# Kernel tuning notes

Measured on AMD Instinct MI355X. Metric: run time of the kernel, lower is better.

## Reference

```python
import jax, jax.numpy as jnp
import numpy as np

T = 1024          # tokens (flattened batch*seq)
H = 1024          # hidden_size
NH = 8            # num_attention_heads
NKV = 4           # num_key_value_heads
HD = H // NH      # head_dim = 128
E = 32            # n_routed_experts
TOPK = 4          # num_experts_per_tok
NG = 8            # n_group
TKG = 4           # topk_group
MI = 512          # moe_intermediate_size
SI = MI * 2       # shared experts intermediate (n_shared_experts=2)
THETA = 10000.0
EPS = 1e-6
RSF = 2.5         # routed_scaling_factor


def setup_inputs() -> dict:
    key = jax.random.key(0)
    ks = jax.random.split(key, 16)
    s = jnp.float32(0.02)
    def nrm(k, shape):
        return jax.random.normal(k, shape, jnp.float32) * s
    return {
        "hidden_states": jax.random.normal(ks[0], (T, H), jnp.float32),
        "position_ids": jnp.arange(T, dtype=jnp.int32),
        "ln1_w": jnp.ones((H,), jnp.float32),
        "ln2_w": jnp.ones((H,), jnp.float32),
        "q_w": nrm(ks[1], (H, H)),            # torch Linear layout [out, in]
        "k_w": nrm(ks[2], (NKV * HD, H)),
        "v_w": nrm(ks[3], (NKV * HD, H)),
        "o_w": nrm(ks[4], (H, H)),
        "router_w": nrm(ks[5], (E, H)),
        "router_bias": jnp.zeros((E,), jnp.float32),  # e_score_correction_bias
        "eg_w": nrm(ks[6], (E, H, MI)),       # expert gate_proj, [E, in, out]
        "eu_w": nrm(ks[7], (E, H, MI)),       # expert up_proj
        "ed_w": nrm(ks[8], (E, MI, H)),       # expert down_proj
        "sg_w": nrm(ks[9], (H, SI)),          # shared experts gate_proj, [in, out]
        "su_w": nrm(ks[10], (H, SI)),
        "sd_w": nrm(ks[11], (SI, H)),
    }


def rmsnorm(x, w):
    var = jnp.mean(x * x, axis=-1, keepdims=True)
    return x * jax.lax.rsqrt(var + EPS) * w


def apply_rope(x, pos):
    # x: [T, heads, HD], non-interleaved (half-rotation)
    half = HD // 2
    inv_freq = 1.0 / (THETA ** (jnp.arange(half, dtype=jnp.float32) / half))
    freqs = pos.astype(jnp.float32)[:, None] * inv_freq[None, :]  # [T, half]
    cos = jnp.cos(freqs)[:, None, :]
    sin = jnp.sin(freqs)[:, None, :]
    x1, x2 = x[..., :half], x[..., half:]
    return jnp.concatenate([x1 * cos - x2 * sin, x2 * cos + x1 * sin], axis=-1)


def attention(h, pos, q_w, k_w, v_w, o_w):
    q = (h @ q_w.T).reshape(T, NH, HD)
    k = (h @ k_w.T).reshape(T, NKV, HD)
    v = (h @ v_w.T).reshape(T, NKV, HD)
    q = apply_rope(q, pos)
    k = apply_rope(k, pos)
    rep = NH // NKV
    k = jnp.repeat(k, rep, axis=1)  # [T, NH, HD]
    v = jnp.repeat(v, rep, axis=1)
    scale = 1.0 / np.sqrt(HD).astype(np.float32)
    scores = jnp.einsum("qhd,khd->hqk", q, k) * scale  # [NH, T, T]
    causal = jnp.tril(jnp.ones((T, T), bool))
    scores = jnp.where(causal[None], scores, jnp.finfo(scores.dtype).min)
    probs = jax.nn.softmax(scores, axis=-1)
    out = jnp.einsum("hqk,khd->qhd", probs, v).reshape(T, H)
    return out @ o_w.T


def router(x, router_w, router_bias):
    logits = x.astype(jnp.float32) @ router_w.T  # [T, E]
    scores = jax.nn.sigmoid(logits)
    sfc = scores + router_bias[None, :]
    # group-limited routing: sum of top-2 per group
    group_scores = jax.lax.top_k(sfc.reshape(T, NG, E // NG), 2)[0].sum(-1)  # [T, NG]
    gidx = jax.lax.top_k(group_scores, TKG)[1]  # [T, TKG]
    gmask = jnp.zeros((T, NG), jnp.float32).at[jnp.arange(T)[:, None], gidx].set(1.0)
    smask = jnp.repeat(gmask, E // NG, axis=1) > 0  # [T, E]
    masked = jnp.where(smask, sfc, 0.0)
    topk_idx = jax.lax.top_k(masked, TOPK)[1]  # [T, TOPK]
    topk_w = jnp.take_along_axis(scores, topk_idx, axis=1)
    topk_w = topk_w / (topk_w.sum(-1, keepdims=True) + 1e-20)  # norm_topk_prob
    return topk_idx, topk_w * RSF


def moe(x, router_w, router_bias, eg_w, eu_w, ed_w, sg_w, su_w, sd_w):
    topk_idx, topk_w = router(x, router_w, router_bias)
    # combine weights [T, E]
    cw = jnp.zeros((T, E), jnp.float32).at[jnp.arange(T)[:, None], topk_idx].add(topk_w)
    g = jnp.einsum("th,ehi->eti", x, eg_w)
    u = jnp.einsum("th,ehi->eti", x, eu_w)
    a = jax.nn.silu(g) * u
    o = jnp.einsum("eti,eih->eth", a, ed_w)
    routed = jnp.einsum("eth,te->th", o, cw)
    shared = (jax.nn.silu(x @ sg_w) * (x @ su_w)) @ sd_w
    return routed + shared


def reference(hidden_states, position_ids, ln1_w, ln2_w, q_w, k_w, v_w, o_w,
              router_w, router_bias, eg_w, eu_w, ed_w, sg_w, su_w, sd_w):
    res = hidden_states
    h = rmsnorm(hidden_states, ln1_w)
    h = attention(h, position_ids, q_w, k_w, v_w, o_w)
    h = res + h
    res = h
    h = rmsnorm(h, ln2_w)
    h = moe(h, router_w, router_bias, eg_w, eu_w, ed_w, sg_w, su_w, sd_w)
    return h + res
```

## Files before the change

### kernel.cpp

```cpp
#include <hip/hip_runtime.h>
#include <math.h>

#define T 1024
#define H 1024
#define NH 8
#define NKV 4
#define HD 128
#define NE 32
#define TOPK 4
#define NG 8
#define MI 512
#define SI 1024
#define RSF 2.5f
#define EPS 1e-6f

#define ASPLIT 4
#define SPLITK 256
#define NPSLOT 40

typedef short bf16x8 __attribute__((ext_vector_type(8)));
typedef float f32x4 __attribute__((ext_vector_type(4)));
#define MFMA16(a, b, c) __builtin_amdgcn_mfma_f32_16x16x32_bf16((a), (b), (c), 0, 0, 0)

__device__ inline unsigned short f2bf(float x) {
    unsigned u = __float_as_uint(x);
    u += 0x7fff + ((u >> 16) & 1);
    return (unsigned short)(u >> 16);
}
__device__ inline float bf2f(unsigned short h) { return __uint_as_float(((unsigned)h) << 16); }

__device__ __host__ inline int cqb_of(int qb) {
    int a = qb >> 2, r = qb & 3;
    return (a + 1) * (2 * a + r);
}

union U16S {
    unsigned short s[16];
    uint4 q[2];
};

__device__ __forceinline__ void gl16(const void* g, void* l) {
    __builtin_amdgcn_global_load_lds((const __attribute__((address_space(1))) unsigned int*)g,
                                     (__attribute__((address_space(3))) unsigned int*)l, 16, 0, 0);
}

__global__ void rmsnorm_split_kernel(const float* __restrict__ x, const float* __restrict__ w,
                                     unsigned short* __restrict__ oh,
                                     unsigned short* __restrict__ ol) {
    int t = blockIdx.x;
    __shared__ float red[256];
    const float* xr = x + (size_t)t * H;
    float s = 0.f;
    for (int i = threadIdx.x; i < H; i += 256) { float v = xr[i]; s += v * v; }
    red[threadIdx.x] = s;
    __syncthreads();
    for (int st = 128; st > 0; st >>= 1) {
        if (threadIdx.x < st) red[threadIdx.x] += red[threadIdx.x + st];
        __syncthreads();
    }
    float inv = rsqrtf(red[0] / (float)H + EPS);
    for (int i = threadIdx.x; i < H; i += 256) {
        float v = xr[i] * inv * w[i];
        unsigned short hb = f2bf(v);
        oh[(size_t)t * H + i] = hb;
        ol[(size_t)t * H + i] = f2bf(v - bf2f(hb));
    }
}

__global__ void rmsnorm_dual_kernel(const float* __restrict__ x, const float* __restrict__ w,
                                    float* __restrict__ outf, unsigned short* __restrict__ outb) {
    int t = blockIdx.x;
    __shared__ float red[256];
    const float* xr = x + (size_t)t * H;
    float s = 0.f;
    for (int i = threadIdx.x; i < H; i += 256) { float v = xr[i]; s += v * v; }
    red[threadIdx.x] = s;
    __syncthreads();
    for (int st = 128; st > 0; st >>= 1) {
        if (threadIdx.x < st) red[threadIdx.x] += red[threadIdx.x + st];
        __syncthreads();
    }
    float inv = rsqrtf(red[0] / (float)H + EPS);
    for (int i = threadIdx.x; i < H; i += 256) {
        float v = xr[i] * inv * w[i];
        outf[(size_t)t * H + i] = v;
        outb[(size_t)t * H + i] = f2bf(v);
    }
}

__global__ void split_w4(const float* __restrict__ qw, const float* __restrict__ kw,
                         const float* __restrict__ vw, const float* __restrict__ ow,
                         unsigned short* __restrict__ qh, unsigned short* __restrict__ ql,
                         unsigned short* __restrict__ kh, unsigned short* __restrict__ kl,
                         unsigned short* __restrict__ vh, unsigned short* __restrict__ vl,
                         unsigned short* __restrict__ oh, unsigned short* __restrict__ ol) {
    int z = blockIdx.z;
    const float* src;
    unsigned short *dh, *dl;
    int n;
    if (z == 0) { src = qw; dh = qh; dl = ql; n = H * H; }
    else if (z == 1) { src = kw; dh = kh; dl = kl; n = NKV * HD * H; }
    else if (z == 2) { src = vw; dh = vh; dl = vl; n = NKV * HD * H; }
    else { src = ow; dh = oh; dl = ol; n = H * H; }
    int i = (blockIdx.x * 256 + threadIdx.x) * 4;
    if (i >= n) return;
    float4 val = *(const float4*)&src[i];
    float vv[4] = {val.x, val.y, val.z, val.w};
    unsigned short hs[4], ls[4];
#pragma unroll
    for (int j = 0; j < 4; ++j) {
        hs[j] = f2bf(vv[j]);
        ls[j] = f2bf(vv[j] - bf2f(hs[j]));
    }
    uint2 hp, lp;
    hp.x = (unsigned)hs[0] | ((unsigned)hs[1] << 16);
    hp.y = (unsigned)hs[2] | ((unsigned)hs[3] << 16);
    lp.x = (unsigned)ls[0] | ((unsigned)ls[1] << 16);
    lp.y = (unsigned)ls[2] | ((unsigned)ls[3] << 16);
    *(uint2*)&dh[i] = hp;
    *(uint2*)&dl[i] = lp;
}

__global__ __launch_bounds__(256) void transpose_cvt(const float* __restrict__ W,
                                                     unsigned short* __restrict__ Wt, int K,
                                                     int N, int eoff) {
    int zl = blockIdx.z;
    const float* src = W + (size_t)(eoff + zl) * K * N;
    unsigned short* dst = Wt + (size_t)zl * K * N;
    int k0 = blockIdx.y * 64, n0 = blockIdx.x * 64;
    __shared__ unsigned short Ls[64][70];
    int tid = threadIdx.x;
    int nn = (tid & 15) * 4, kr = tid >> 4;
#pragma unroll
    for (int p = 0; p < 4; ++p) {
        int k = kr + p * 16;
        float4 v = *(const float4*)&src[(size_t)(k0 + k) * N + n0 + nn];
        Ls[k][nn] = f2bf(v.x);
        Ls[k][nn + 1] = f2bf(v.y);
        Ls[k][nn + 2] = f2bf(v.z);
        Ls[k][nn + 3] = f2bf(v.w);
    }
    __syncthreads();
    int n = tid >> 2, kq = (tid & 3) * 16;
    U16S o;
#pragma unroll
    for (int j = 0; j < 16; ++j) o.s[j] = Ls[kq + j][n];
    unsigned short* drow = dst + (size_t)(n0 + n) * K + k0 + kq;
    *(uint4*)drow = o.q[0];
    *(uint4*)(drow + 8) = o.q[1];
}

__global__ __launch_bounds__(256) void vt_split(const float* __restrict__ vb,
                                                unsigned short* __restrict__ VTh,
                                                unsigned short* __restrict__ VTl) {
    int t0 = blockIdx.x * 64, c0 = blockIdx.y * 64;
    __shared__ unsigned short Hs[64][70], Lsh[64][70];
    int tid = threadIdx.x;
    int nn = (tid & 15) * 4, kr = tid >> 4;
#pragma unroll
    for (int p = 0; p < 4; ++p) {
        int t = kr + p * 16;
        float4 v = *(const float4*)&vb[(size_t)(t0 + t) * (NKV * HD) + c0 + nn];
        float vv[4] = {v.x, v.y, v.z, v.w};
#pragma unroll
        for (int j = 0; j < 4; ++j) {
            unsigned short hb = f2bf(vv[j]);
            Hs[t][nn + j] = hb;
            Lsh[t][nn + j] = f2bf(vv[j] - bf2f(hb));
        }
    }
    __syncthreads();
    int n = tid >> 2, kq = (tid & 3) * 16;
    U16S oh, ol;
#pragma unroll
    for (int j = 0; j < 16; ++j) {
        oh.s[j] = Hs[kq + j][n];
        ol.s[j] = Lsh[kq + j][n];
    }
    size_t drow = (size_t)(c0 + n) * T + t0 + kq;
    *(uint4*)&VTh[drow] = oh.q[0];
    *(uint4*)&VTh[drow + 8] = oh.q[1];
    *(uint4*)&VTl[drow] = ol.q[0];
    *(uint4*)&VTl[drow + 8] = ol.q[1];
}

__global__ __launch_bounds__(256) void router_logits_kernel(const float* __restrict__ x,
                                                            const float* __restrict__ W,
                                                            float* __restrict__ logits) {
    int t = blockIdx.x;
    __shared__ float xs[H];
    int tid = threadIdx.x;
    *(float4*)&xs[tid * 4] = *(const float4*)&x[(size_t)t * H + tid * 4];
    __syncthreads();
    int e = tid >> 3, p = tid & 7;
    const float* wr = W + (size_t)e * H;
    float s = 0.f;
#pragma unroll
    for (int i = 0; i < 32; ++i) {
        int k = i * 32 + p * 4;
        float4 wv = *(const float4*)&wr[k];
        float4 xv = *(const float4*)&xs[k];
        s += wv.x * xv.x + wv.y * xv.y + wv.z * xv.z + wv.w * xv.w;
    }
#pragma unroll
    for (int off = 1; off < 8; off <<= 1) s += __shfl_xor(s, off);
    if (p == 0) logits[(size_t)t * NE + e] = s;
}

__global__ __launch_bounds__(256) void gemm3_qkv(
    const unsigned short* __restrict__ Xh, const unsigned short* __restrict__ Xl,
    const unsigned short* __restrict__ Wqh, const unsigned short* __restrict__ Wql,
    const unsigned short* __restrict__ Wkh, const unsigned short* __restrict__ Wkl,
    const unsigned short* __restrict__ Wvh, const unsigned short* __restrict__ Wvl,
    float* __restrict__ qo, float* __restrict__ ko, float* __restrict__ vo) {
    __shared__ short Ahs[2][128][32], Als[2][128][32], Bhs[2][64][32], Bls[2][64][32];
    int tid = threadIdx.x;
    int m0 = blockIdx.y * 128;
    int n0 = blockIdx.x * 64;
    const unsigned short *Wh, *Wl;
    float* O;
    int ldo, nc0;
    if (n0 < 1024) { nc0 = n0; Wh = Wqh; Wl = Wql; O = qo; ldo = H; }
    else if (n0 < 1536) { nc0 = n0 - 1024; Wh = Wkh; Wl = Wkl; O = ko; ldo = NKV * HD; }
    else { nc0 = n0 - 1536; Wh = Wvh; Wl = Wvl; O = vo; ldo = NKV * HD; }
    int wave = tid >> 6, lane = tid & 63;
    int lr = lane & 15, lq = lane >> 4;
    int wm = (wave >> 1) * 64, wn = (wave & 1) * 32;
    int srow = lane >> 2, skb = (lane & 3) * 8;
    const unsigned short *ah_p[2], *al_p[2];
#pragma unroll
    for (int p = 0; p < 2; ++p) {
        int m = m0 + wave * 32 + p * 16 + srow;
        ah_p[p] = Xh + (size_t)m * H + skb;
        al_p[p] = Xl + (size_t)m * H + skb;
    }
    int bn = nc0 + wave * 16 + srow;
    const unsigned short* bh_p = Wh + (size_t)bn * H + skb;
    const unsigned short* bl_p = Wl + (size_t)bn * H + skb;
    f32x4 acc[4][2];
#pragma unroll
    for (int i = 0; i < 4; ++i)
#pragma unroll
        for (int j = 0; j < 2; ++j) acc[i][j] = (f32x4){0.f, 0.f, 0.f, 0.f};
    for (int k0 = 0; k0 < H; k0 += 64) {
#pragma unroll
        for (int c = 0; c < 2; ++c) {
            int kc = k0 + c * 32;
#pragma unroll
            for (int p = 0; p < 2; ++p) {
                gl16(ah_p[p] + kc, &Ahs[c][wave * 32 + p * 16 + srow][skb]);
                gl16(al_p[p] + kc, &Als[c][wave * 32 + p * 16 + srow][skb]);
            }
            gl16(bh_p + kc, &Bhs[c][wave * 16 + srow][skb]);
            gl16(bl_p + kc, &Bls[c][wave * 16 + srow][skb]);
        }
        __syncthreads();
#pragma unroll
        for (int c = 0; c < 2; ++c) {
            bf16x8 a_h[4], a_l[4], b_h[2], b_l[2];
#pragma unroll
            for (int mt = 0; mt < 4; ++mt) {
                a_h[mt] = *(const bf16x8*)&Ahs[c][wm + mt * 16 + lr][lq * 8];
                a_l[mt] = *(const bf16x8*)&Als[c][wm + mt * 16 + lr][lq * 8];
            }
#pragma unroll
            for (int nt = 0; nt < 2; ++nt) {
                b_h[nt] = *(const bf16x8*)&Bhs[c][wn + nt * 16 + lr][lq * 8];
                b_l[nt] = *(const bf16x8*)&Bls[c][wn + nt * 16 + lr][lq * 8];
            }
#pragma unroll
            for (int mt = 0; mt < 4; ++mt)
#pragma unroll
                for (int nt = 0; nt < 2; ++nt) {
                    acc[mt][nt] = MFMA16(a_h[mt], b_h[nt], acc[mt][nt]);
                    acc[mt][nt] = MFMA16(a_h[mt], b_l[nt], acc[mt][nt]);
                    acc[mt][nt] = MFMA16(a_l[mt], b_h[nt], acc[mt][nt]);
                }
        }
        __syncthreads();
    }
#pragma unroll
    for (int mt = 0; mt < 4; ++mt)
#pragma unroll
        for (int nt = 0; nt < 2; ++nt)
#pragma unroll
            for (int p = 0; p < 4; ++p) {
                int m = m0 + wm + mt * 16 + lq * 4 + p;
                int col = nc0 + wn + nt * 16 + lr;
                O[(size_t)m * ldo + col] = acc[mt][nt][p];
            }
}

__global__ __launch_bounds__(256) void gemm3_res(
    const unsigned short* __restrict__ Agh, const unsigned short* __restrict__ Agl,
    const unsigned short* __restrict__ Wh, const unsigned short* __restrict__ Wl,
    const float* __restrict__ res, float* __restrict__ O) {
    __shared__ short Ahs[2][128][32], Als[2][128][32], Bhs[2][64][32], Bls[2][64][32];
    int tid = threadIdx.x;
    int m0 = blockIdx.y * 128;
    int n0 = blockIdx.x * 64;
    int wave = tid >> 6, lane = tid & 63;
    int lr = lane & 15, lq = lane >> 4;
    int wm = (wave >> 1) * 64, wn = (wave & 1) * 32;
    int srow = lane >> 2, skb = (lane & 3) * 8;
    const unsigned short *ah_p[2], *al_p[2];
#pragma unroll
    for (int p = 0; p < 2; ++p) {
        int m = m0 + wave * 32 + p * 16 + srow;
        ah_p[p] = Agh + (size_t)m * H + skb;
        al_p[p] = Agl + (size_t)m * H + skb;
    }
    int bn = n0 + wave * 16 + srow;
    const unsigned short* bh_p = Wh + (size_t)bn * H + skb;
    const unsigned short* bl_p = Wl + (size_t)bn * H + skb;
    f32x4 acc[4][2];
#pragma unroll
    for (int i = 0; i < 4; ++i)
#pragma unroll
        for (int j = 0; j < 2; ++j) acc[i][j] = (f32x4){0.f, 0.f, 0.f, 0.f};
    for (int k0 = 0; k0 < H; k0 += 64) {
#pragma unroll
        for (int c = 0; c < 2; ++c) {
            int kc = k0 + c * 32;
#pragma unroll
            for (int p = 0; p < 2; ++p) {
                gl16(ah_p[p] + kc, &Ahs[c][wave * 32 + p * 16 + srow][skb]);
                gl16(al_p[p] + kc, &Als[c][wave * 32 + p * 16 + srow][skb]);
            }
            gl16(bh_p + kc, &Bhs[c][wave * 16 + srow][skb]);
            gl16(bl_p + kc, &Bls[c][wave * 16 + srow][skb]);
        }
        __syncthreads();
#pragma unroll
        for (int c = 0; c < 2; ++c) {
            bf16x8 a_h[4], a_l[4], b_h[2], b_l[2];
#pragma unroll
            for (int mt = 0; mt < 4; ++mt) {
                a_h[mt] = *(const bf16x8*)&Ahs[c][wm + mt * 16 + lr][lq * 8];
                a_l[mt] = *(const bf16x8*)&Als[c][wm + mt * 16 + lr][lq * 8];
            }
#pragma unroll
            for (int nt = 0; nt < 2; ++nt) {
                b_h[nt] = *(const bf16x8*)&Bhs[c][wn + nt * 16 + lr][lq * 8];
                b_l[nt] = *(const bf16x8*)&Bls[c][wn + nt * 16 + lr][lq * 8];
            }
#pragma unroll
            for (int mt = 0; mt < 4; ++mt)
#pragma unroll
                for (int nt = 0; nt < 2; ++nt) {
                    acc[mt][nt] = MFMA16(a_h[mt], b_h[nt], acc[mt][nt]);
                    acc[mt][nt] = MFMA16(a_h[mt], b_l[nt], acc[mt][nt]);
                    acc[mt][nt] = MFMA16(a_l[mt], b_h[nt], acc[mt][nt]);
                }
        }
        __syncthreads();
    }
#pragma unroll
    for (int mt = 0; mt < 4; ++mt)
#pragma unroll
        for (int nt = 0; nt < 2; ++nt)
#pragma unroll
            for (int p = 0; p < 4; ++p) {
                int m = m0 + wm + mt * 16 + lq * 4 + p;
                int col = n0 + wn + nt * 16 + lr;
                O[(size_t)m * H + col] = res[(size_t)m * H + col] + acc[mt][nt][p];
            }
}

__global__ void rope_kernel(float* __restrict__ q, const float* __restrict__ k,
                            const int* __restrict__ pos, unsigned short* __restrict__ Khg,
                            unsigned short* __restrict__ Klg) {
    int i = blockIdx.x * 256 + threadIdx.x;
    const int totq = T * NH * 64;
    const int tot = totq + T * NKV * 64;
    if (i >= tot) return;
    if (i < totq) {
        int r = i;
        int d = r & 63; r >>= 6;
        int hh = r % NH, t = r / NH;
        float p = (float)pos[t];
        float inv = powf(10000.0f, -(float)d / 64.0f);
        float fr = p * inv;
        float sv, cv;
        sincosf(fr, &sv, &cv);
        size_t bi = ((size_t)t * NH + hh) * HD + d;
        float x1 = q[bi], x2 = q[bi + 64];
        q[bi] = x1 * cv - x2 * sv;
        q[bi + 64] = x2 * cv + x1 * sv;
    } else {
        int r = i - totq;
        int d = r & 63; r >>= 6;
        int hh = r % NKV, t = r / NKV;
        float p = (float)pos[t];
        float inv = powf(10000.0f, -(float)d / 64.0f);
        float fr = p * inv;
        float sv, cv;
        sincosf(fr, &sv, &cv);
        size_t bi = ((size_t)t * NKV + hh) * HD + d;
        float x1 = k[bi], x2 = k[bi + 64];
        float n1 = x1 * cv - x2 * sv;
        float n2 = x2 * cv + x1 * sv;
        unsigned short h1 = f2bf(n1), h2b = f2bf(n2);
        Khg[bi] = h1;
        Khg[bi + 64] = h2b;
        Klg[bi] = f2bf(n1 - bf2f(h1));
        Klg[bi + 64] = f2bf(n2 - bf2f(h2b));
    }
}

#define KS_LD 136
#define VS_LD 40
#define PS_LD 34
__global__ __launch_bounds__(256) void attn_split(const float* __restrict__ Q,
                                                  const unsigned short* __restrict__ Khg,
                                                  const unsigned short* __restrict__ Klg,
                                                  const unsigned short* __restrict__ VTh,
                                                  const unsigned short* __restrict__ VTl,
                                                  float* __restrict__ po,
                                                  float* __restrict__ pm,
                                                  float* __restrict__ pl) {
    int h = blockIdx.x;
    int qb = blockIdx.y;
    int sp = blockIdx.z;
    int kvh = h >> 1;
    int q0 = qb * 64;
    int kend = q0 + 64;
    int ks = sp * SPLITK;
    if (ks >= kend) return;
    int ke = min(ks + SPLITK, kend);
    __shared__ __attribute__((aligned(16))) short Ksh[32][KS_LD], Ksl[32][KS_LD];
    __shared__ __attribute__((aligned(16))) short Vsh[128][VS_LD], Vsl[128][VS_LD];
    __shared__ short Ph[4][16][PS_LD], Pl[4][16][PS_LD];
    int tid = threadIdx.x;
    int wave = tid >> 6, lane = tid & 63;
    int lr = lane & 15, lq = lane >> 4;
    const float scale = 0.08838834764831845f;

    bf16x8 qh[4], ql[4];
    {
        const float* qrow = Q + (size_t)(q0 + wave * 16 + lr) * H + h * HD;
#pragma unroll
        for (int c = 0; c < 4; ++c) {
            float4 v0 = *(const float4*)(qrow + c * 32 + lq * 8);
            float4 v1 = *(const float4*)(qrow + c * 32 + lq * 8 + 4);
            float vv[8] = {v0.x, v0.y, v0.z, v0.w, v1.x, v1.y, v1.z, v1.w};
#pragma unroll
            for (int j = 0; j < 8; ++j) {
                unsigned short hb = f2bf(vv[j]);
                qh[c][j] = (short)hb;
                ql[c][j] = (short)f2bf(vv[j] - bf2f(hb));
            }
        }
    }
    f32x4 o[8];
#pragma unroll
    for (int nt = 0; nt < 8; ++nt) o[nt] = (f32x4){0.f, 0.f, 0.f, 0.f};
    float m_r[4] = {-1e30f, -1e30f, -1e30f, -1e30f};
    float l_r[4] = {0.f, 0.f, 0.f, 0.f};

    int kts = ks >> 5, kte = ke >> 5;
    int ntw = ((q0 + wave * 16 + 15) >> 5) + 1;

    int key_k = tid >> 3, kc = (tid & 7) * 16;
    int d_v = tid >> 1, vc = (tid & 1) * 16;
    const unsigned short* kbase_h = Khg + (size_t)kvh * HD + kc;
    const unsigned short* kbase_l = Klg + (size_t)kvh * HD + kc;
    const unsigned short* vbase_h = VTh + (size_t)(kvh * HD + d_v) * T + vc;
    const unsigned short* vbase_l = VTl + (size_t)(kvh * HD + d_v) * T + vc;

    uint4 kr0, kr1, kr2, kr3, vr0, vr1, vr2, vr3;
#define LOADT(KT)                                                                    \
    {                                                                                \
        size_t koff = (size_t)((KT)*32 + key_k) * (NKV * HD);                        \
        kr0 = *(const uint4*)(kbase_h + koff);                                       \
        kr1 = *(const uint4*)(kbase_h + koff + 8);                                   \
        kr2 = *(const uint4*)(kbase_l + koff);                                       \
        kr3 = *(const uint4*)(kbase_l + koff + 8);                                   \
        int voff = (KT)*32;                                                          \
        vr0 = *(const uint4*)(vbase_h + voff);                                       \
        vr1 = *(const uint4*)(vbase_h + voff + 8);                                   \
        vr2 = *(const uint4*)(vbase_l + voff);                                       \
        vr3 = *(const uint4*)(vbase_l + voff + 8);                                   \
    }

    LOADT(kts);
    for (int kt = kts; kt < kte; ++kt) {
        int k0 = kt * 32;
        __syncthreads();
        *(uint4*)&Ksh[key_k][kc] = kr0;
        *(uint4*)&Ksh[key_k][kc + 8] = kr1;
        *(uint4*)&Ksl[key_k][kc] = kr2;
        *(uint4*)&Ksl[key_k][kc + 8] = kr3;
        *(uint4*)&Vsh[d_v][vc] = vr0;
        *(uint4*)&Vsh[d_v][vc + 8] = vr1;
        *(uint4*)&Vsl[d_v][vc] = vr2;
        *(uint4*)&Vsl[d_v][vc + 8] = vr3;
        __syncthreads();
        if (kt + 1 < kte) LOADT(kt + 1);
        if (kt < ntw) {
            f32x4 s[2];
            s[0] = (f32x4){0.f, 0.f, 0.f, 0.f};
            s[1] = (f32x4){0.f, 0.f, 0.f, 0.f};
#pragma unroll
            for (int nt = 0; nt < 2; ++nt)
#pragma unroll
                for (int c = 0; c < 4; ++c) {
                    bf16x8 kh = *(const bf16x8*)&Ksh[nt * 16 + lr][c * 32 + lq * 8];
                    bf16x8 kl = *(const bf16x8*)&Ksl[nt * 16 + lr][c * 32 + lq * 8];
                    s[nt] = MFMA16(qh[c], kh, s[nt]);
                    s[nt] = MFMA16(ql[c], kh, s[nt]);
                    s[nt] = MFMA16(qh[c], kl, s[nt]);
                }
            int gr_base = q0 + wave * 16 + lq * 4;
#pragma unroll
            for (int nt = 0; nt < 2; ++nt) {
                int gc = k0 + nt * 16 + lr;
#pragma unroll
                for (int p = 0; p < 4; ++p) {
                    float sv = s[nt][p] * scale;
                    if (gc > gr_base + p) sv = -1e30f;
                    s[nt][p] = sv;
                }
            }
            float alpha[4];
#pragma unroll
            for (int p = 0; p < 4; ++p) {
                float mx = fmaxf(s[0][p], s[1][p]);
#pragma unroll
                for (int off = 1; off < 16; off <<= 1) mx = fmaxf(mx, __shfl_xor(mx, off));
                float mn = fmaxf(m_r[p], mx);
                alpha[p] = __expf(m_r[p] - mn);
                float p0 = __expf(s[0][p] - mn);
                float p1 = __expf(s[1][p] - mn);
                float ps = p0 + p1;
#pragma unroll
                for (int off = 1; off < 16; off <<= 1) ps += __shfl_xor(ps, off);
                l_r[p] = l_r[p] * alpha[p] + ps;
                m_r[p] = mn;
                int r = lq * 4 + p;
                unsigned short h0 = f2bf(p0);
                Ph[wave][r][lr] = (short)h0;
                Pl[wave][r][lr] = (short)f2bf(p0 - bf2f(h0));
                unsigned short h1 = f2bf(p1);
                Ph[wave][r][lr + 16] = (short)h1;
                Pl[wave][r][lr + 16] = (short)f2bf(p1 - bf2f(h1));
            }
            bf16x8 pah = *(const bf16x8*)&Ph[wave][lr][lq * 8];
            bf16x8 pal = *(const bf16x8*)&Pl[wave][lr][lq * 8];
#pragma unroll
            for (int nt = 0; nt < 8; ++nt) {
#pragma unroll
                for (int p = 0; p < 4; ++p) o[nt][p] *= alpha[p];
                bf16x8 vh = *(const bf16x8*)&Vsh[nt * 16 + lr][lq * 8];
                bf16x8 vl = *(const bf16x8*)&Vsl[nt * 16 + lr][lq * 8];
                o[nt] = MFMA16(pah, vh, o[nt]);
                o[nt] = MFMA16(pal, vh, o[nt]);
                o[nt] = MFMA16(pah, vl, o[nt]);
            }
        }
    }
#undef LOADT
    int pbase = h * NPSLOT + cqb_of(qb) + sp;
    float* porow = po + (size_t)pbase * (64 * 128);
#pragma unroll
    for (int nt = 0; nt < 8; ++nt)
#pragma unroll
        for (int p = 0; p < 4; ++p) {
            int row = wave * 16 + lq * 4 + p;
            porow[row * 128 + nt * 16 + lr] = o[nt][p];
        }
    if (lr == 0) {
#pragma unroll
        for (int p = 0; p < 4; ++p) {
            int row = wave * 16 + lq * 4 + p;
            pm[(size_t)pbase * 64 + row] = m_r[p];
            pl[(size_t)pbase * 64 + row] = l_r[p];
        }
    }
}

__global__ __launch_bounds__(256) void attn_merge(const float* __restrict__ po,
                                                  const float* __restrict__ pm,
                                                  const float* __restrict__ pl,
                                                  unsigned short* __restrict__ Oh,
                                                  unsigned short* __restrict__ Ol) {
    int h = blockIdx.x, qb = blockIdx.y;
    int nact = qb / 4 + 1;
    int tid = threadIdx.x;
    int row = tid >> 2;
    int c0 = (tid & 3) * 32;
    int pb = h * NPSLOT + cqb_of(qb);
    float ms[ASPLIT], ws[ASPLIT];
    float mstar = -1e30f;
#pragma unroll
    for (int s = 0; s < ASPLIT; ++s)
        if (s < nact) {
            ms[s] = pm[(size_t)(pb + s) * 64 + row];
            mstar = fmaxf(mstar, ms[s]);
        }
    float lstar = 0.f;
#pragma unroll
    for (int s = 0; s < ASPLIT; ++s)
        if (s < nact) {
            ws[s] = __expf(ms[s] - mstar);
            lstar += ws[s] * pl[(size_t)(pb + s) * 64 + row];
        }
    float linv = 1.f / lstar;
    size_t obase = (size_t)(qb * 64 + row) * H + h * HD + c0;
#pragma unroll
    for (int j = 0; j < 32; j += 4) {
        float acc[4] = {0.f, 0.f, 0.f, 0.f};
#pragma unroll
        for (int s = 0; s < ASPLIT; ++s)
            if (s < nact) {
                float4 v =
                    *(const float4*)&po[(size_t)(pb + s) * (64 * 128) + row * 128 + c0 + j];
                acc[0] += ws[s] * v.x;
                acc[1] += ws[s] * v.y;
                acc[2] += ws[s] * v.z;
                acc[3] += ws[s] * v.w;
            }
#pragma unroll
        for (int q = 0; q < 4; ++q) {
            float v = acc[q] * linv;
            unsigned short hb = f2bf(v);
            Oh[obase + j + q] = hb;
            Ol[obase + j + q] = f2bf(v - bf2f(hb));
        }
    }
}

__global__ void router_kernel(const float* __restrict__ logits, const float* __restrict__ bias,
                              int* __restrict__ topk_idx, float* __restrict__ topkw) {
    int t = blockIdx.x * 256 + threadIdx.x;
    if (t >= T) return;
    float sc[NE], sfc[NE];
    for (int e = 0; e < NE; ++e) {
        float s = 1.f / (1.f + expf(-logits[(size_t)t * NE + e]));
        sc[e] = s;
        sfc[e] = s + bias[e];
    }
    float gs[NG];
    for (int g = 0; g < NG; ++g) {
        float m1 = -1e30f, m2 = -1e30f;
        for (int i = 0; i < 4; ++i) {
            float v = sfc[g * 4 + i];
            if (v > m1) { m2 = m1; m1 = v; }
            else if (v > m2) m2 = v;
        }
        gs[g] = m1 + m2;
    }
    bool gmask[NG];
    for (int g = 0; g < NG; ++g) gmask[g] = false;
    for (int r = 0; r < 4; ++r) {
        int bi = 0; float bv = -1e30f;
        for (int g = 0; g < NG; ++g)
            if (gs[g] > bv) { bv = gs[g]; bi = g; }
        gmask[bi] = true;
        gs[bi] = -1e30f;
    }
    float msfc[NE];
    for (int e = 0; e < NE; ++e) msfc[e] = gmask[e >> 2] ? sfc[e] : 0.f;
    int idx[TOPK]; float w[TOPK]; float wsum = 0.f;
    for (int r = 0; r < TOPK; ++r) {
        int bi = 0; float bv = -1e30f;
        for (int e = 0; e < NE; ++e)
            if (msfc[e] > bv) { bv = msfc[e]; bi = e; }
        idx[r] = bi;
        msfc[bi] = -1e30f;
        w[r] = sc[bi];
        wsum += w[r];
    }
    float inv = RSF / (wsum + 1e-20f);
    for (int r = 0; r < TOPK; ++r) {
        topk_idx[(size_t)t * TOPK + r] = idx[r];
        topkw[(size_t)t * TOPK + r] = w[r] * inv;
    }
}

__global__ void bucket_kernel(const int* __restrict__ topk_idx, int* __restrict__ counts,
                              int* __restrict__ offs, int* __restrict__ tok_of,
                              int* __restrict__ slot_of) {
    __shared__ int cnt[NE], off[NE], fil[NE];
    int tid = threadIdx.x;
    if (tid < NE) { cnt[tid] = 0; fil[tid] = 0; }
    __syncthreads();
    for (int i = tid; i < T * TOPK; i += 256) atomicAdd(&cnt[topk_idx[i]], 1);
    __syncthreads();
    if (tid == 0) {
        int a = 0;
        for (int e = 0; e < NE; ++e) { off[e] = a; a += cnt[e]; }
    }
    __syncthreads();
    if (tid < NE) { counts[tid] = cnt[tid]; offs[tid] = off[tid]; }
    for (int i = tid; i < T * TOPK; i += 256) {
        int e = topk_idx[i];
        int p = off[e] + atomicAdd(&fil[e], 1);
        tok_of[p] = i >> 2;
        slot_of[i] = p;
    }
}

__global__ __launch_bounds__(256) void up_mfma2(
    const unsigned short* __restrict__ Xb, const unsigned short* __restrict__ Gt,
    const unsigned short* __restrict__ Ut, size_t wstride, const int* __restrict__ tok_of,
    const int* __restrict__ offs, const int* __restrict__ counts, int eoff,
    unsigned short* __restrict__ outb, int ldo) {
    int zl = blockIdx.z;
    int e = eoff + zl;
    int cnt = counts ? counts[e] : T;
    int base = offs ? offs[e] : 0;
    int m0 = blockIdx.y * 128;
    if (m0 >= cnt) return;
    int n0 = blockIdx.x * 64;
    const unsigned short* gt = Gt + (size_t)zl * wstride;
    const unsigned short* ut = Ut + (size_t)zl * wstride;
    __shared__ short As[2][128][32];
    __shared__ short Gs[2][64][32];
    __shared__ short Us[2][64][32];
    __shared__ int toks[128];
    int tid = threadIdx.x;
    if (tid < 128) {
        int m = m0 + tid;
        if (m >= cnt) m = cnt - 1;
        toks[tid] = tok_of ? tok_of[base + m] : m;
    }
    __syncthreads();
    int wave = tid >> 6, lane = tid & 63;
    int lr = lane & 15, lq = lane >> 4;
    int wm = (wave >> 1) * 64, wn = (wave & 1) * 32;
    int srow = lane >> 2, skb = (lane & 3) * 8;
    const unsigned short* aptr[2];
#pragma unroll
    for (int p = 0; p < 2; ++p)
        aptr[p] = Xb + (size_t)toks[wave * 32 + p * 16 + srow] * H + skb;
    const unsigned short* gptr = gt + (size_t)(n0 + wave * 16 + srow) * H + skb;
    const unsigned short* uptr = ut + (size_t)(n0 + wave * 16 + srow) * H + skb;
    f32x4 ag[4][2], au[4][2];
#pragma unroll
    for (int i = 0; i < 4; ++i)
#pragma unroll
        for (int j = 0; j < 2; ++j) {
            ag[i][j] = (f32x4){0.f, 0.f, 0.f, 0.f};
            au[i][j] = (f32x4){0.f, 0.f, 0.f, 0.f};
        }
    for (int k0 = 0; k0 < H; k0 += 64) {
#pragma unroll
        for (int c = 0; c < 2; ++c) {
            int kc = k0 + c * 32;
#pragma unroll
            for (int p = 0; p < 2; ++p)
                gl16(aptr[p] + kc, &As[c][wave * 32 + p * 16 + srow][skb]);
            gl16(gptr + kc, &Gs[c][wave * 16 + srow][skb]);
            gl16(uptr + kc, &Us[c][wave * 16 + srow][skb]);
        }
        __syncthreads();
#pragma unroll
        for (int c = 0; c < 2; ++c) {
            bf16x8 a[4], gg[2], uu[2];
#pragma unroll
            for (int mt = 0; mt < 4; ++mt)
                a[mt] = *(const bf16x8*)&As[c][wm + mt * 16 + lr][lq * 8];
#pragma unroll
            for (int nt = 0; nt < 2; ++nt) {
                gg[nt] = *(const bf16x8*)&Gs[c][wn + nt * 16 + lr][lq * 8];
                uu[nt] = *(const bf16x8*)&Us[c][wn + nt * 16 + lr][lq * 8];
            }
#pragma unroll
            for (int mt = 0; mt < 4; ++mt)
#pragma unroll
                for (int nt = 0; nt < 2; ++nt) {
                    ag[mt][nt] = MFMA16(a[mt], gg[nt], ag[mt][nt]);
                    au[mt][nt] = MFMA16(a[mt], uu[nt], au[mt][nt]);
                }
        }
        __syncthreads();
    }
#pragma unroll
    for (int mt = 0; mt < 4; ++mt)
#pragma unroll
        for (int nt = 0; nt < 2; ++nt)
#pragma unroll
            for (int p = 0; p < 4; ++p) {
                int m = m0 + wm + mt * 16 + lq * 4 + p;
                if (m >= cnt) continue;
                int orow = tok_of ? base + m : m;
                int col = n0 + wn + nt * 16 + lr;
                float gv = ag[mt][nt][p], uv = au[mt][nt][p];
                float sv = gv / (1.f + __expf(-gv)) * uv;
                outb[(size_t)orow * ldo + col] = f2bf(sv);
            }
}

__global__ __launch_bounds__(256) void down_mfma2(const unsigned short* __restrict__ Ab, int K,
                                                  const unsigned short* __restrict__ Wt,
                                                  size_t wstride, const int* __restrict__ offs,
                                                  const int* __restrict__ counts, int eoff,
                                                  float* __restrict__ Co) {
    int zl = blockIdx.z;
    int e = eoff + zl;
    int cnt = counts ? counts[e] : T;
    int base = offs ? offs[e] : 0;
    int m0 = blockIdx.y * 128;
    if (m0 >= cnt) return;
    int n0 = blockIdx.x * 128;
    const unsigned short* wt = Wt + (size_t)zl * wstride;
    __shared__ short As[2][128][32];
    __shared__ short Bs[2][128][32];
    int tid = threadIdx.x;
    int wave = tid >> 6, lane = tid & 63;
    int lr = lane & 15, lq = lane >> 4;
    int wm = (wave >> 1) * 64, wn = (wave & 1) * 64;
    int srow = lane >> 2, skb = (lane & 3) * 8;
    const unsigned short* aptr[2];
    const unsigned short* bptr[2];
#pragma unroll
    for (int p = 0; p < 2; ++p) {
        int m = m0 + wave * 32 + p * 16 + srow;
        if (m >= cnt) m = cnt - 1;
        aptr[p] = Ab + (size_t)(base + m) * K + skb;
        bptr[p] = wt + (size_t)(n0 + wave * 32 + p * 16 + srow) * K + skb;
    }
    f32x4 acc[4][4];
#pragma unroll
    for (int i = 0; i < 4; ++i)
#pragma unroll
        for (int j = 0; j < 4; ++j) acc[i][j] = (f32x4){0.f, 0.f, 0.f, 0.f};
    for (int k0 = 0; k0 < K; k0 += 64) {
#pragma unroll
        for (int c = 0; c < 2; ++c) {
            int kc = k0 + c * 32;
#pragma unroll
            for (int p = 0; p < 2; ++p) {
                gl16(aptr[p] + kc, &As[c][wave * 32 + p * 16 + srow][skb]);
                gl16(bptr[p] + kc, &Bs[c][wave * 32 + p * 16 + srow][skb]);
            }
        }
        __syncthreads();
#pragma unroll
        for (int c = 0; c < 2; ++c) {
            bf16x8 a[4], b[4];
#pragma unroll
            for (int mt = 0; mt < 4; ++mt)
                a[mt] = *(const bf16x8*)&As[c][wm + mt * 16 + lr][lq * 8];
#pragma unroll
            for (int nt = 0; nt < 4; ++nt)
                b[nt] = *(const bf16x8*)&Bs[c][wn + nt * 16 + lr][lq * 8];
#pragma unroll
            for (int mt = 0; mt < 4; ++mt)
#pragma unroll
                for (int nt = 0; nt < 4; ++nt) acc[mt][nt] = MFMA16(a[mt], b[nt], acc[mt][nt]);
        }
        __syncthreads();
    }
#pragma unroll
    for (int mt = 0; mt < 4; ++mt)
#pragma unroll
        for (int nt = 0; nt < 4; ++nt)
#pragma unroll
            for (int p = 0; p < 4; ++p) {
                int m = m0 + wm + mt * 16 + lq * 4 + p;
                if (m >= cnt) continue;
                int col = n0 + wn + nt * 16 + lr;
                Co[(size_t)(base + m) * H + col] = acc[mt][nt][p];
            }
}

__global__ void combine_kernel(const float* __restrict__ o_slot, const int* __restrict__ slot_of,
                               const float* __restrict__ topkw, const float* __restrict__ h2,
                               const float* __restrict__ sharedo, float* __restrict__ out) {
    int t = blockIdx.x;
    int d = threadIdx.x * 4;
    float4 a = *(const float4*)&h2[(size_t)t * H + d];
    float4 b = *(const float4*)&sharedo[(size_t)t * H + d];
    float4 acc = make_float4(a.x + b.x, a.y + b.y, a.z + b.z, a.w + b.w);
#pragma unroll
    for (int r = 0; r < TOPK; ++r) {
        int s = slot_of[t * TOPK + r];
        float w = topkw[t * TOPK + r];
        float4 v = *(const float4*)&o_slot[(size_t)s * H + d];
        acc.x += w * v.x; acc.y += w * v.y; acc.z += w * v.z; acc.w += w * v.w;
    }
    *(float4*)&out[(size_t)t * H + d] = acc;
}

extern "C" void kernel_launch(void* const* d_in, const int* in_sizes, int n_in,
                              void* d_out, int out_size, void* d_ws, size_t ws_size,
                              hipStream_t stream) {
    const float* hidden = (const float*)d_in[0];
    const int* pos = (const int*)d_in[1];
    const float* ln1w = (const float*)d_in[2];
    const float* ln2w = (const float*)d_in[3];
    const float* q_w = (const float*)d_in[4];
    const float* k_w = (const float*)d_in[5];
    const float* v_w = (const float*)d_in[6];
    const float* o_w = (const float*)d_in[7];
    const float* router_w = (const float*)d_in[8];
    const float* router_b = (const float*)d_in[9];
    const float* eg_w = (const float*)d_in[10];
    const float* eu_w = (const float*)d_in[11];
    const float* ed_w = (const float*)d_in[12];
    const float* sg_w = (const float*)d_in[13];
    const float* su_w = (const float*)d_in[14];
    const float* sd_w = (const float*)d_in[15];
    float* out = (float*)d_out;

    float* f = (float*)d_ws;
    float* xslot = f;   f += (size_t)T * H;
    float* qb = f;      f += (size_t)T * H;
    float* kb = f;      f += (size_t)T * NKV * HD;
    float* vb = f;      f += (size_t)T * NKV * HD;
    float* aoslot = f;  f += (size_t)T * H;
    float* ext = f;     f += (size_t)4 * 1024 * 1024;
    float* h2 = f;      f += (size_t)T * H;
    float* h_ln2f = f;  f += (size_t)T * H;
    float* logits = f;  f += (size_t)T * NE;
    float* topkw = f;   f += (size_t)T * TOPK;
    float* o_slot = f;  f += (size_t)T * TOPK * H;
    float* sharedo = f; f += (size_t)T * H;
    unsigned short* h_ln2b = (unsigned short*)f;
    unsigned short* abuf = h_ln2b + (size_t)T * H;
    unsigned short* ashared = abuf + (size_t)T * TOPK * MI;
    int* topk_idx = (int*)(ashared + (size_t)T * SI);
    int* counts = topk_idx + T * TOPK;
    int* fills = counts + NE;
    int* offs = fills + NE;
    int* tok_of = offs + NE;
    int* slot_of = tok_of + T * TOPK;
    (void)fills;

    unsigned short* wT = (unsigned short*)((char*)d_ws + (size_t)80 * 1024 * 1024);
    unsigned short* egTall = wT;
    unsigned short* euTall = egTall + (size_t)NE * H * MI;
    unsigned short* edTall = euTall + (size_t)NE * H * MI;
    bool big_ws = ws_size >= (size_t)(80 + 96 + 1) * 1024 * 1024;

    unsigned short* We = (unsigned short*)ext;
    const size_t HH = (size_t)H * H;
    const size_t KH = (size_t)NKV * HD * H;
    unsigned short* Wqh = We;
    unsigned short* Wql = Wqh + HH;
    unsigned short* Wkh = Wql + HH;
    unsigned short* Wkl = Wkh + KH;
    unsigned short* Wvh = Wkl + KH;
    unsigned short* Wvl = Wvh + KH;
    unsigned short* Woh = Wvl + KH;
    unsigned short* Wol = Woh + HH;

    unsigned short* Xh = (unsigned short*)xslot;
    unsigned short* Xl = Xh + (size_t)T * H;
    unsigned short* Aoh = (unsigned short*)aoslot;
    unsigned short* Aol = Aoh + (size_t)T * H;

    unsigned short* Khg = (unsigned short*)xslot;
    unsigned short* Klg = Khg + (size_t)T * NKV * HD;
    unsigned short* VTh = Klg + (size_t)T * NKV * HD;
    unsigned short* VTl = VTh + (size_t)T * NKV * HD;

    float* attn_po = o_slot;
    float* attn_pm = (float*)abuf;
    float* attn_pl = attn_pm + (size_t)NH * NPSLOT * 64;

    unsigned short* arena = (unsigned short*)xslot;
    unsigned short* egT = arena;
    unsigned short* euT = arena + (size_t)16 * H * MI;
    unsigned short* edT = arena;
    unsigned short* sgT = arena;
    unsigned short* suT = arena + (size_t)H * SI;
    unsigned short* sdT = arena;

    dim3 b256(256);

    split_w4<<<dim3(HH / (256 * 4), 1, 4), b256, 0, stream>>>(q_w, k_w, v_w, o_w, Wqh, Wql,
                                                              Wkh, Wkl, Wvh, Wvl, Woh, Wol);
    rmsnorm_split_kernel<<<T, b256, 0, stream>>>(hidden, ln1w, Xh, Xl);

    gemm3_qkv<<<dim3(32, 8), b256, 0, stream>>>(Xh, Xl, Wqh, Wql, Wkh, Wkl, Wvh, Wvl,
                                                qb, kb, vb);
    {
        int tot = T * NH * 64 + T * NKV * 64;
        rope_kernel<<<(tot + 255) / 256, b256, 0, stream>>>(qb, kb, pos, Khg, Klg);
    }
    vt_split<<<dim3(T / 64, (NKV * HD) / 64), b256, 0, stream>>>(vb, VTh, VTl);
    attn_split<<<dim3(NH, T / 64, ASPLIT), b256, 0, stream>>>(qb, Khg, Klg, VTh, VTl,
                                                              attn_po, attn_pm, attn_pl);
    attn_merge<<<dim3(NH, T / 64), b256, 0, stream>>>(attn_po, attn_pm, attn_pl, Aoh, Aol);
    gemm3_res<<<dim3(16, 8), b256, 0, stream>>>(Aoh, Aol, Woh, Wol, hidden, h2);
    rmsnorm_dual_kernel<<<T, b256, 0, stream>>>(h2, ln2w, h_ln2f, h_ln2b);

    router_logits_kernel<<<T, b256, 0, stream>>>(h_ln2f, router_w, logits);
    router_kernel<<<(T + 255) / 256, b256, 0, stream>>>(logits, router_b, topk_idx, topkw);
    bucket_kernel<<<1, b256, 0, stream>>>(topk_idx, counts, offs, tok_of, slot_of);

    if (big_ws) {
        transpose_cvt<<<dim3(MI / 64, H / 64, NE), b256, 0, stream>>>(eg_w, egTall, H, MI, 0);
        transpose_cvt<<<dim3(MI / 64, H / 64, NE), b256, 0, stream>>>(eu_w, euTall, H, MI, 0);
        up_mfma2<<<dim3(MI / 64, 8, NE), b256, 0, stream>>>(
            h_ln2b, egTall, euTall, (size_t)H * MI, tok_of, offs, counts, 0, abuf, MI);
        transpose_cvt<<<dim3(H / 64, MI / 64, NE), b256, 0, stream>>>(ed_w, edTall, MI, H, 0);
        down_mfma2<<<dim3(H / 128, 8, NE), b256, 0, stream>>>(
            abuf, MI, edTall, (size_t)MI * H, offs, counts, 0, o_slot);
    } else {
        for (int g = 0; g < 2; ++g) {
            int eo = g * 16;
            transpose_cvt<<<dim3(MI / 64, H / 64, 16), b256, 0, stream>>>(eg_w, egT, H, MI, eo);
            transpose_cvt<<<dim3(MI / 64, H / 64, 16), b256, 0, stream>>>(eu_w, euT, H, MI, eo);
            up_mfma2<<<dim3(MI / 64, 8, 16), b256, 0, stream>>>(
                h_ln2b, egT, euT, (size_t)H * MI, tok_of, offs, counts, eo, abuf, MI);
        }
        for (int g = 0; g < 2; ++g) {
            int eo = g * 16;
            transpose_cvt<<<dim3(H / 64, MI / 64, 16), b256, 0, stream>>>(ed_w, edT, MI, H, eo);
            down_mfma2<<<dim3(H / 128, 8, 16), b256, 0, stream>>>(
                abuf, MI, edT, (size_t)MI * H, offs, counts, eo, o_slot);
        }
    }
    transpose_cvt<<<dim3(SI / 64, H / 64, 1), b256, 0, stream>>>(sg_w, sgT, H, SI, 0);
    transpose_cvt<<<dim3(SI / 64, H / 64, 1), b256, 0, stream>>>(su_w, suT, H, SI, 0);
    up_mfma2<<<dim3(SI / 64, T / 128, 1), b256, 0, stream>>>(
        h_ln2b, sgT, suT, 0, nullptr, nullptr, nullptr, 0, ashared, SI);
    transpose_cvt<<<dim3(H / 64, SI / 64, 1), b256, 0, stream>>>(sd_w, sdT, SI, H, 0);
    down_mfma2<<<dim3(H / 128, T / 128, 1), b256, 0, stream>>>(
        ashared, SI, sdT, 0, nullptr, nullptr, 0, sharedo);

    combine_kernel<<<T, b256, 0, stream>>>(o_slot, slot_of, topkw, h2, sharedo, out);
}
```

Before: 533.2 us.

## Register-prefetch next K tile and pad LDS rows in expert GEMMs

In the routed-expert up (gate/up+SiLU) and down GEMM kernels, the direct global-to-LDS loads are replaced by register prefetch. The next K tile is loaded into registers while the current tile's MFMAs run, then written to LDS between barriers. LDS rows are padded from 32 to 40 shorts to reduce bank conflicts on the fragment reads. This costs extra VGPRs, which may lower occupancy, and adds a store pass through LDS in place of the direct async copy.

Measured after the change: 517.8 us. 1.03x faster.

```diff
diff --git a/kernel.cpp b/kernel.cpp
--- a/kernel.cpp
+++ b/kernel.cpp
@@ -17,6 +17,8 @@
 #define ASPLIT 4
 #define SPLITK 256
 #define NPSLOT 40
+
+#define KP 40
 
 typedef short bf16x8 __attribute__((ext_vector_type(8)));
 typedef float f32x4 __attribute__((ext_vector_type(4)));
@@ -715,9 +717,9 @@
     int n0 = blockIdx.x * 64;
     const unsigned short* gt = Gt + (size_t)zl * wstride;
     const unsigned short* ut = Ut + (size_t)zl * wstride;
-    __shared__ short As[2][128][32];
-    __shared__ short Gs[2][64][32];
-    __shared__ short Us[2][64][32];
+    __shared__ __attribute__((aligned(16))) short As[2][128][KP];
+    __shared__ __attribute__((aligned(16))) short Gs[2][64][KP];
+    __shared__ __attribute__((aligned(16))) short Us[2][64][KP];
     __shared__ int toks[128];
     int tid = threadIdx.x;
     if (tid < 128) {
@@ -744,17 +746,31 @@
             ag[i][j] = (f32x4){0.f, 0.f, 0.f, 0.f};
             au[i][j] = (f32x4){0.f, 0.f, 0.f, 0.f};
         }
+    uint4 ra00, ra01, ra10, ra11, rg0, rg1, ru0, ru1;
+#define LOADU(K0)                                          \
+    {                                                      \
+        ra00 = *(const uint4*)(aptr[0] + (K0));            \
+        ra01 = *(const uint4*)(aptr[1] + (K0));            \
+        ra10 = *(const uint4*)(aptr[0] + (K0) + 32);       \
+        ra11 = *(const uint4*)(aptr[1] + (K0) + 32);       \
+        rg0 = *(const uint4*)(gptr + (K0));                \
+        rg1 = *(const uint4*)(gptr + (K0) + 32);           \
+        ru0 = *(const uint4*)(uptr + (K0));                \
+        ru1 = *(const uint4*)(uptr + (K0) + 32);           \
+    }
+    LOADU(0);
     for (int k0 = 0; k0 < H; k0 += 64) {
-#pragma unroll
-        for (int c = 0; c < 2; ++c) {
-            int kc = k0 + c * 32;
-#pragma unroll
-            for (int p = 0; p < 2; ++p)
-                gl16(aptr[p] + kc, &As[c][wave * 32 + p * 16 + srow][skb]);
-            gl16(gptr + kc, &Gs[c][wave * 16 + srow][skb]);
-            gl16(uptr + kc, &Us[c][wave * 16 + srow][skb]);
-        }
-        __syncthreads();
+        __syncthreads();
+        *(uint4*)&As[0][wave * 32 + srow][skb] = ra00;
+        *(uint4*)&As[0][wave * 32 + 16 + srow][skb] = ra01;
+        *(uint4*)&As[1][wave * 32 + srow][skb] = ra10;
+        *(uint4*)&As[1][wave * 32 + 16 + srow][skb] = ra11;
+        *(uint4*)&Gs[0][wave * 16 + srow][skb] = rg0;
+        *(uint4*)&Gs[1][wave * 16 + srow][skb] = rg1;
+        *(uint4*)&Us[0][wave * 16 + srow][skb] = ru0;
+        *(uint4*)&Us[1][wave * 16 + srow][skb] = ru1;
+        __syncthreads();
+        if (k0 + 64 < H) LOADU(k0 + 64);
 #pragma unroll
         for (int c = 0; c < 2; ++c) {
             bf16x8 a[4], gg[2], uu[2];
@@ -774,8 +790,8 @@
                     au[mt][nt] = MFMA16(a[mt], uu[nt], au[mt][nt]);
                 }
         }
-        __syncthreads();
-    }
+    }
+#undef LOADU
 #pragma unroll
     for (int mt = 0; mt < 4; ++mt)
 #pragma unroll
@@ -805,8 +821,8 @@
     if (m0 >= cnt) return;
     int n0 = blockIdx.x * 128;
     const unsigned short* wt = Wt + (size_t)zl * wstride;
-    __shared__ short As[2][128][32];
-    __shared__ short Bs[2][128][32];
+    __shared__ __attribute__((aligned(16))) short As[2][128][KP];
+    __shared__ __attribute__((aligned(16))) short Bs[2][128][KP];
     int tid = threadIdx.x;
     int wave = tid >> 6, lane = tid & 63;
     int lr = lane & 15, lq = lane >> 4;
@@ -826,17 +842,31 @@
     for (int i = 0; i < 4; ++i)
 #pragma unroll
         for (int j = 0; j < 4; ++j) acc[i][j] = (f32x4){0.f, 0.f, 0.f, 0.f};
+    uint4 ra00, ra01, ra10, ra11, rb00, rb01, rb10, rb11;
+#define LOADD(K0)                                          \
+    {                                                      \
+        ra00 = *(const uint4*)(aptr[0] + (K0));            \
+        ra01 = *(const uint4*)(aptr[1] + (K0));            \
+        ra10 = *(const uint4*)(aptr[0] + (K0) + 32);       \
+        ra11 = *(const uint4*)(aptr[1] + (K0) + 32);       \
+        rb00 = *(const uint4*)(bptr[0] + (K0));            \
+        rb01 = *(const uint4*)(bptr[1] + (K0));            \
+        rb10 = *(const uint4*)(bptr[0] + (K0) + 32);       \
+        rb11 = *(const uint4*)(bptr[1] + (K0) + 32);       \
+    }
+    LOADD(0);
     for (int k0 = 0; k0 < K; k0 += 64) {
-#pragma unroll
-        for (int c = 0; c < 2; ++c) {
-            int kc = k0 + c * 32;
-#pragma unroll
-            for (int p = 0; p < 2; ++p) {
-                gl16(aptr[p] + kc, &As[c][wave * 32 + p * 16 + srow][skb]);
-                gl16(bptr[p] + kc, &Bs[c][wave * 32 + p * 16 + srow][skb]);
-            }
-        }
-        __syncthreads();
+        __syncthreads();
+        *(uint4*)&As[0][wave * 32 + srow][skb] = ra00;
+        *(uint4*)&As[0][wave * 32 + 16 + srow][skb] = ra01;
+        *(uint4*)&As[1][wave * 32 + srow][skb] = ra10;
+        *(uint4*)&As[1][wave * 32 + 16 + srow][skb] = ra11;
+        *(uint4*)&Bs[0][wave * 32 + srow][skb] = rb00;
+        *(uint4*)&Bs[0][wave * 32 + 16 + srow][skb] = rb01;
+        *(uint4*)&Bs[1][wave * 32 + srow][skb] = rb10;
+        *(uint4*)&Bs[1][wave * 32 + 16 + srow][skb] = rb11;
+        __syncthreads();
+        if (k0 + 64 < K) LOADD(k0 + 64);
 #pragma unroll
         for (int c = 0; c < 2; ++c) {
             bf16x8 a[4], b[4];
@@ -851,8 +881,8 @@
 #pragma unroll
                 for (int nt = 0; nt < 4; ++nt) acc[mt][nt] = MFMA16(a[mt], b[nt], acc[mt][nt]);
         }
-        __syncthreads();
-    }
+    }
+#undef LOADD
 #pragma unroll
     for (int mt = 0; mt < 4; ++mt)
 #pragma unroll
```
